# Performance work log

Measured on AMD Instinct MI355X. Metric: run time of the kernel, lower is better.

Reference implementation:

```python
import jax, jax.numpy as jnp
import numpy as np

PAD = 32  # integer padding from init_kwargs

def _conv1d_fft(x, weight, bias):
    # x: (B, Cin, L), weight: (Cout, Cin, K), bias: (Cout,)
    B, Cin, L = x.shape
    Cout, _, K = weight.shape
    p = PAD
    padded = (L + 2 * p + 31) & ~31          # round up to multiple of 32
    out_len = 2 * p + L - (K - 1)
    offset = (min(K, L) - 1) // 2 - p
    roll = -((K - 1) // 2) + offset
    # pad kernel to padded length then circularly roll (centers the kernel)
    k_pad = jnp.pad(weight, ((0, 0), (0, 0), (0, padded - K)))
    k_rolled = jnp.roll(k_pad, roll, axis=-1)
    x_fft = jnp.fft.rfft(x, n=padded, axis=-1)          # (B, Cin, F)
    k_fft = jnp.fft.rfft(k_rolled, axis=-1)             # (Cout, Cin, F)
    # multiply-reduce over in_channels == batched complex GEMM over freq bins
    b_fft = jnp.einsum('bif,oif->bof', x_fft, jnp.conj(k_fft))
    # bias enters only the DC bin, scaled by padded length (irfft normalization)
    b_fft = b_fft.at[..., 0].add(bias.astype(b_fft.dtype) * padded)
    b = jnp.fft.irfft(b_fft, n=padded, axis=-1)
    return b[..., :out_len]


def setup_inputs() -> dict:
    key = jax.random.key(0)
    k1, k2, k3 = jax.random.split(key, 3)
    B, Cin, Cout, L, K = 16, 128, 128, 4096, 129
    stdv = 1.0 / np.sqrt(Cin * K)
    x = jax.random.normal(k1, (B, Cin, L), dtype=jnp.float32)
    weight = jax.random.uniform(k2, (Cout, Cin, K), dtype=jnp.float32, minval=-stdv, maxval=stdv)
    bias = jax.random.uniform(k3, (Cout,), dtype=jnp.float32, minval=-stdv, maxval=stdv)
    return {"x": x, "weight": weight, "bias": bias}


def reference(x, weight, bias):
    return _conv1d_fft(x, weight, bias)
```

## Files before the change

### kernel.cpp

```cpp
#include <hip/hip_runtime.h>


typedef _Float16 f16;
typedef _Float16 f16x8 __attribute__((ext_vector_type(8)));
typedef float f32x4 __attribute__((ext_vector_type(4)));

#define NB   16
#define CI   128
#define CO   128
#define LIN  4096
#define KW   129
#define TOUT 4032
#define UPAD 4224
#define XT_BYTES ((size_t)NB * UPAD * CI * 2)
#define WLDS 32768

__device__ __forceinline__ void gld16(void* lds, const void* g) {
    __builtin_amdgcn_global_load_lds(
        (const __attribute__((address_space(1))) unsigned int*)g,
        (__attribute__((address_space(3))) unsigned int*)lds,
        16, 0, 0);
}

__global__ __launch_bounds__(256) void xt_prep(const float* __restrict__ x,
                                               f16* __restrict__ xt) {
    __shared__ float tile[128][33];
    const int b  = blockIdx.y;
    const int u0 = blockIdx.x * 32;
    const int l0 = u0 - 32;
    const int tid = threadIdx.x;
    const int col = tid & 31;
    const int cib = tid >> 5;
#pragma unroll
    for (int r = 0; r < 16; ++r) {
        int ci = cib + r * 8;
        int l  = l0 + col;
        float v = 0.f;
        if (l >= 0 && l < LIN) v = x[((size_t)b * CI + ci) * LIN + l];
        tile[ci][col] = v;
    }
    __syncthreads();
#pragma unroll
    for (int it = 0; it < 2; ++it) {
        int idx  = tid + it * 256;
        int ur   = idx >> 4;
        int slot = idx & 15;
        int c    = slot ^ ((u0 + ur) & 7);
        f16x8 v;
#pragma unroll
        for (int j = 0; j < 8; ++j) v[j] = (f16)tile[c * 8 + j][ur];
        *(f16x8*)(&xt[((size_t)b * UPAD + u0 + ur) * CI + slot * 8]) = v;
    }
}

__global__ __launch_bounds__(256) void wt_prep(const float* __restrict__ w,
                                               f16* __restrict__ wt) {
    __shared__ float tile[32][132];
    const int cic = blockIdx.x;
    const int co  = blockIdx.y;
    const int ci0 = cic * 32;
    const int tid = threadIdx.x;
    for (int it = 0; it < 17; ++it) {
        int idx = tid + it * 256;
        if (idx < 32 * 129) {
            int i = idx / 129;
            int m = idx - i * 129;
            tile[i][m] = w[(size_t)co * (CI * KW) + (size_t)(ci0 + i) * KW + m];
        }
    }
    __syncthreads();
    const int swz = (co >> 1) & 3;
    for (int it = 0; it < 3; ++it) {
        int idx = tid + it * 256;
        if (idx < 129 * 4) {
            int m = idx >> 2;
            int c = idx & 3;
            int kk = m * 4 + cic;
            int slot = c ^ swz;
            f16x8 v;
#pragma unroll
            for (int j = 0; j < 8; ++j) v[j] = (f16)tile[c * 8 + j][m];
            *(f16x8*)(&wt[((size_t)kk * 128 + co) * 32 + slot * 8]) = v;
        }
    }
}

__global__ __launch_bounds__(256, 2) void conv_main(
    const f16* __restrict__ xt, const f16* __restrict__ wt,
    const float* __restrict__ bias, float* __restrict__ out)
{
    extern __shared__ char smem[];
    const int tid  = threadIdx.x;
    const int lane = tid & 63;
    const int wid  = tid >> 6;
    const int l15  = lane & 15;
    const int l4   = lane >> 4;
    const int wco  = (wid >> 1) << 6;
    const int wtt  = (wid & 1) << 6;

    const int tt = blockIdx.x;
    const int b  = blockIdx.y;
    const int u0 = tt << 7;

    const char* xbase = (const char*)xt + ((size_t)b * UPAD + u0) * (CI * 2);
    const char* wbase = (const char*)wt;

    const int aslotx = (l4 ^ ((l15 >> 1) & 3)) << 4;
    int aoff[4];
#pragma unroll
    for (int ct = 0; ct < 4; ++ct)
        aoff[ct] = ((wco + ct * 16 + l15) << 6) + aslotx;

    int brow[4];
#pragma unroll
    for (int st = 0; st < 4; ++st)
        brow[st] = wtt + st * 16 + l15;

    f32x4 acc[4][4];
#pragma unroll
    for (int i = 0; i < 4; ++i)
#pragma unroll
        for (int j = 0; j < 4; ++j)
            acc[i][j] = (f32x4){0.f, 0.f, 0.f, 0.f};

    for (int p = 0; p < 2; ++p) {
        const int pbase = 2 * p;

        __builtin_amdgcn_s_barrier();
#pragma unroll
        for (int i = 0; i < 8; ++i) {
            int off   = tid * 16 + i * 4096;
            int row   = off >> 7;
            int inrow = off & 127;
            gld16(smem + off, xbase + row * 256 + p * 128 + inrow);
        }
        {
            const char* wsrc = wbase + (size_t)pbase * 8192;
            gld16(smem + WLDS + tid * 16,        wsrc + tid * 16);
            gld16(smem + WLDS + 4096 + tid * 16, wsrc + 4096 + tid * 16);
        }
        asm volatile("s_waitcnt vmcnt(0)" ::: "memory");
        __builtin_amdgcn_s_barrier();

        auto kstep = [&](int s, int rb, int pb, bool pf) {
            if (pf) {
                const int sp = s + 1;
                const int kk = (sp >> 1) * 4 + pbase + (sp & 1);
                const char* wsrc = wbase + (size_t)kk * 8192;
                gld16(smem + WLDS + pb * 8192 + tid * 16,        wsrc + tid * 16);
                gld16(smem + WLDS + pb * 8192 + 4096 + tid * 16, wsrc + 4096 + tid * 16);
                asm volatile("s_waitcnt vmcnt(2)" ::: "memory");
            } else {
                asm volatile("s_waitcnt vmcnt(0)" ::: "memory");
            }
            __builtin_amdgcn_s_barrier();

            const int m  = s >> 1;
            const int cl = ((s & 1) << 2) + l4;
            const char* wlds = smem + WLDS + rb * 8192;
            f16x8 af[4], bf[4];
#pragma unroll
            for (int ct = 0; ct < 4; ++ct)
                af[ct] = *(const f16x8*)(wlds + aoff[ct]);
#pragma unroll
            for (int st = 0; st < 4; ++st) {
                int row  = brow[st] + m;
                int slot = cl ^ (row & 7);
                bf[st] = *(const f16x8*)(smem + (row << 7) + (slot << 4));
            }
#pragma unroll
            for (int ct = 0; ct < 4; ++ct)
#pragma unroll
                for (int st = 0; st < 4; ++st)
                    acc[ct][st] = __builtin_amdgcn_mfma_f32_16x16x32_f16(
                        af[ct], bf[st], acc[ct][st], 0, 0, 0);
        };

        for (int g = 0; g < 85; ++g) {
            int s = g * 3;
            kstep(s,     0, 1, true);
            kstep(s + 1, 1, 2, true);
            kstep(s + 2, 2, 0, true);
        }
        kstep(255, 0, 1, true);
        kstep(256, 1, 2, true);
        kstep(257, 2, 0, false);
    }

#pragma unroll
    for (int ct = 0; ct < 4; ++ct) {
#pragma unroll
        for (int r = 0; r < 4; ++r) {
            int co = wco + ct * 16 + l4 * 4 + r;
            float bv = bias[co];
            float* orow = out + ((size_t)b * CO + co) * TOUT;
#pragma unroll
            for (int st = 0; st < 4; ++st) {
                int t = u0 + wtt + st * 16 + l15;
                if (t < TOUT) orow[t] = acc[ct][st][r] + bv;
            }
        }
    }
}

extern "C" void kernel_launch(void* const* d_in, const int* in_sizes, int n_in,
                              void* d_out, int out_size, void* d_ws, size_t ws_size,
                              hipStream_t stream) {
    const float* x    = (const float*)d_in[0];
    const float* w    = (const float*)d_in[1];
    const float* bias = (const float*)d_in[2];
    float* out = (float*)d_out;

    f16* xt = (f16*)d_ws;
    f16* wt = (f16*)((char*)d_ws + XT_BYTES);

    xt_prep<<<dim3(UPAD / 32, NB), 256, 0, stream>>>(x, xt);
    wt_prep<<<dim3(4, CO), 256, 0, stream>>>(w, wt);
    conv_main<<<dim3(32, NB), 256, 57344, stream>>>(xt, wt, bias, out);
}
```

Measured before the change: 329.4 us.

## Deepen weight LDS ring to four slots and double-buffer MFMA fragments

The weight staging ring in LDS grows from three to four 8 KB slots, so weight tiles are prefetched three k-steps ahead instead of one. A/B fragments for the next k-step are now read from LDS into a second register set before the barrier, so the MFMAs for the current step run from registers after it. The goal is to hide global-load and LDS-read latency behind the matrix ops and drop the barrier at the top of each pass. In exchange it uses more LDS per block (64 KB) and more VGPRs for the duplicate fragments, which could hurt occupancy under the two-blocks launch bound.

Measured after the change: 318.8 us. 1.03x faster.

```diff
diff --git a/kernel.cpp b/kernel.cpp
--- a/kernel.cpp
+++ b/kernel.cpp
@@ -104,6 +104,7 @@
 
     const char* xbase = (const char*)xt + ((size_t)b * UPAD + u0) * (CI * 2);
     const char* wbase = (const char*)wt;
+    char* wring = smem + WLDS;
 
     const int aslotx = (l4 ^ ((l15 >> 1) & 3)) << 4;
     int aoff[4];
@@ -126,7 +127,6 @@
     for (int p = 0; p < 2; ++p) {
         const int pbase = 2 * p;
 
-        __builtin_amdgcn_s_barrier();
 #pragma unroll
         for (int i = 0; i < 8; ++i) {
             int off   = tid * 16 + i * 4096;
@@ -134,57 +134,68 @@
             int inrow = off & 127;
             gld16(smem + off, xbase + row * 256 + p * 128 + inrow);
         }
-        {
-            const char* wsrc = wbase + (size_t)pbase * 8192;
-            gld16(smem + WLDS + tid * 16,        wsrc + tid * 16);
-            gld16(smem + WLDS + 4096 + tid * 16, wsrc + 4096 + tid * 16);
-        }
-        asm volatile("s_waitcnt vmcnt(0)" ::: "memory");
+#pragma unroll
+        for (int c = 0; c < 3; ++c) {
+            const int kk = (c >> 1) * 4 + pbase + (c & 1);
+            const char* wsrc = wbase + (size_t)kk * 8192;
+            gld16(wring + c * 8192 + tid * 16,        wsrc + tid * 16);
+            gld16(wring + c * 8192 + 4096 + tid * 16, wsrc + 4096 + tid * 16);
+        }
+        asm volatile("s_waitcnt vmcnt(2)" ::: "memory");
         __builtin_amdgcn_s_barrier();
 
-        auto kstep = [&](int s, int rb, int pb, bool pf) {
-            if (pf) {
-                const int sp = s + 1;
-                const int kk = (sp >> 1) * 4 + pbase + (sp & 1);
+        f16x8 afA[4], bfA[4], afB[4], bfB[4];
+#pragma unroll
+        for (int ct = 0; ct < 4; ++ct)
+            afA[ct] = *(const f16x8*)(wring + aoff[ct]);
+#pragma unroll
+        for (int st = 0; st < 4; ++st) {
+            int row  = brow[st];
+            int slot = l4 ^ (row & 7);
+            bfA[st] = *(const f16x8*)(smem + (row << 7) + (slot << 4));
+        }
+
+        auto body = [&](int j, f16x8 (&afC)[4], f16x8 (&bfC)[4],
+                               f16x8 (&afN)[4], f16x8 (&bfN)[4]) {
+            const bool issue = (j + 3 <= 257);
+            if (issue) {
+                const int kn = j + 3;
+                const int kk = (kn >> 1) * 4 + pbase + (kn & 1);
                 const char* wsrc = wbase + (size_t)kk * 8192;
-                gld16(smem + WLDS + pb * 8192 + tid * 16,        wsrc + tid * 16);
-                gld16(smem + WLDS + pb * 8192 + 4096 + tid * 16, wsrc + 4096 + tid * 16);
-                asm volatile("s_waitcnt vmcnt(2)" ::: "memory");
-            } else {
-                asm volatile("s_waitcnt vmcnt(0)" ::: "memory");
+                char* dst = wring + (kn & 3) * 8192;
+                gld16(dst + tid * 16,        wsrc + tid * 16);
+                gld16(dst + 4096 + tid * 16, wsrc + 4096 + tid * 16);
             }
+            if (j + 1 <= 257) {
+                const int jn  = j + 1;
+                const int mn  = jn >> 1;
+                const int cln = ((jn & 1) << 2) + l4;
+                const char* wl = wring + (jn & 3) * 8192;
+#pragma unroll
+                for (int ct = 0; ct < 4; ++ct)
+                    afN[ct] = *(const f16x8*)(wl + aoff[ct]);
+#pragma unroll
+                for (int st = 0; st < 4; ++st) {
+                    int row  = brow[st] + mn;
+                    int slot = cln ^ (row & 7);
+                    bfN[st] = *(const f16x8*)(smem + (row << 7) + (slot << 4));
+                }
+            }
+            if (issue) asm volatile("s_waitcnt vmcnt(2)" ::: "memory");
+            else       asm volatile("s_waitcnt vmcnt(0)" ::: "memory");
             __builtin_amdgcn_s_barrier();
-
-            const int m  = s >> 1;
-            const int cl = ((s & 1) << 2) + l4;
-            const char* wlds = smem + WLDS + rb * 8192;
-            f16x8 af[4], bf[4];
-#pragma unroll
-            for (int ct = 0; ct < 4; ++ct)
-                af[ct] = *(const f16x8*)(wlds + aoff[ct]);
-#pragma unroll
-            for (int st = 0; st < 4; ++st) {
-                int row  = brow[st] + m;
-                int slot = cl ^ (row & 7);
-                bf[st] = *(const f16x8*)(smem + (row << 7) + (slot << 4));
-            }
 #pragma unroll
             for (int ct = 0; ct < 4; ++ct)
 #pragma unroll
                 for (int st = 0; st < 4; ++st)
                     acc[ct][st] = __builtin_amdgcn_mfma_f32_16x16x32_f16(
-                        af[ct], bf[st], acc[ct][st], 0, 0, 0);
+                        afC[ct], bfC[st], acc[ct][st], 0, 0, 0);
         };
 
-        for (int g = 0; g < 85; ++g) {
-            int s = g * 3;
-            kstep(s,     0, 1, true);
-            kstep(s + 1, 1, 2, true);
-            kstep(s + 2, 2, 0, true);
-        }
-        kstep(255, 0, 1, true);
-        kstep(256, 1, 2, true);
-        kstep(257, 2, 0, false);
+        for (int jj = 0; jj < 258; jj += 2) {
+            body(jj,     afA, bfA, afB, bfB);
+            body(jj + 1, afB, bfB, afA, bfA);
+        }
     }
 
 #pragma unroll
@@ -216,5 +227,5 @@
 
     xt_prep<<<dim3(UPAD / 32, NB), 256, 0, stream>>>(x, xt);
     wt_prep<<<dim3(4, CO), 256, 0, stream>>>(w, wt);
-    conv_main<<<dim3(32, NB), 256, 57344, stream>>>(xt, wt, bias, out);
-}
+    conv_main<<<dim3(32, NB), 256, 65536, stream>>>(xt, wt, bias, out);
+}
```
